# Performance work log

Measured on AMD Instinct MI355X. Metric: run time of the kernel, lower is better.

The kernel has to match this reference:

```python
import jax, jax.numpy as jnp
import numpy as np

B, T, C = 4, 2048, 1024
H, D = 16, 64           # num_heads, head_size
R = D // 2              # rotary_ndims = 32


def _make_rope(T, R):
    # RotaryEmbedding(dim=R): inv_freq over arange(0, R, 2)
    inv_freq = 1.0 / (10000.0 ** (np.arange(0, R, 2, dtype=np.float32) / R))
    t = np.arange(T, dtype=np.float32)
    freqs = np.einsum('i,j->ij', t, inv_freq)        # [T, R/2]
    emb = np.concatenate([freqs, freqs], axis=-1)    # [T, R]
    return jnp.asarray(np.stack([np.cos(emb), np.sin(emb)]), dtype=jnp.float32)  # [2, T, R]


def setup_inputs() -> dict:
    key = jax.random.key(0)
    ks = jax.random.split(key, 10)
    s = 1.0 / np.sqrt(C)
    inp = {
        'x': jax.random.normal(ks[0], (B, T, C), dtype=jnp.float32),
        'RoPE': _make_rope(T, R),
        'key_padding_mask': jax.random.randint(ks[1], (B, T), 0, 2, dtype=jnp.int32),
        'Wq': jax.random.normal(ks[2], (C, C), dtype=jnp.float32) * s,
        'bq': jnp.zeros((C,), dtype=jnp.float32),
        'Wk': jax.random.normal(ks[3], (C, C), dtype=jnp.float32) * s,
        'bk': jnp.zeros((C,), dtype=jnp.float32),
        'Wv': jax.random.normal(ks[4], (C, C), dtype=jnp.float32) * s,
        'bv': jnp.zeros((C,), dtype=jnp.float32),
        'Wo': jax.random.normal(ks[5], (C, C), dtype=jnp.float32) * s,
        'bo': jnp.zeros((C,), dtype=jnp.float32),
    }
    return inp


def _rotate_half(x):
    x1, x2 = x[..., : x.shape[-1] // 2], x[..., x.shape[-1] // 2:]
    return jnp.concatenate([-x2, x1], axis=-1)


def reference(x, RoPE, key_padding_mask, Wq, bq, Wk, bk, Wv, bv, Wo, bo):
    Bx, Tx, Cx = x.shape
    # projections -> [B, H, T, D]
    def proj(W, b):
        return (x @ W.T + b).reshape(Bx, Tx, H, D).transpose(0, 2, 1, 3)
    q, k, v = proj(Wq, bq), proj(Wk, bk), proj(Wv, bv)

    # partial rotary: first R dims rotated, rest passed through
    q_rot, q_pass = q[..., :R], q[..., R:]
    k_rot, k_pass = k[..., :R], k[..., R:]
    cos, sin = RoPE[0][:Tx], RoPE[1][:Tx]            # [T, R]
    q_rot = q_rot * cos + _rotate_half(q_rot) * sin
    k_rot = k_rot * cos + _rotate_half(k_rot) * sin
    q = jnp.concatenate([q_rot, q_pass], axis=-1)
    k = jnp.concatenate([k_rot, k_pass], axis=-1)

    att = jnp.einsum('bhqd,bhkd->bhqk', q, k) * (1.0 / np.sqrt(D))
    mask = key_padding_mask[:, None, None, :]        # [B,1,1,T]
    att = jnp.where(mask == 0, jnp.asarray(-1e30, att.dtype), att)
    att = jax.nn.softmax(att, axis=-1)
    out = jnp.einsum('bhqk,bhkd->bhqd', att, v)      # [B,H,T,D]
    out = out.transpose(0, 2, 1, 3).reshape(Bx, Tx, Cx)
    return out @ Wo.T + bo
```

## Files before the change

kernel.cpp:

```cpp
#include <hip/hip_runtime.h>
#include <stdint.h>


typedef __attribute__((ext_vector_type(8))) short bf16x8;
typedef __attribute__((ext_vector_type(4))) float f32x4;
typedef __attribute__((ext_vector_type(4))) short short4v;
typedef __attribute__((ext_vector_type(2))) uint32_t uint2v;

#define MFMA16(a, b, c) __builtin_amdgcn_mfma_f32_16x16x32_bf16((a), (b), (c), 0, 0, 0)

#if __has_builtin(__builtin_amdgcn_exp2f)
#define FEXP(x) __builtin_amdgcn_exp2f(x)
#define QSCALE 0.18033688011112042f
#else
#define FEXP(x) __expf(x)
#define QSCALE 0.125f
#endif

static __device__ __forceinline__ short f2bf(float f) {
  union { float fv; uint32_t u; } v; v.fv = f;
  uint32_t r = v.u + 0x7FFFu + ((v.u >> 16) & 1u);
  return (short)(r >> 16);
}

static __device__ __forceinline__ uint32_t pack_trunc(float a, float b) {
  union { float f; uint32_t u; } ua, ub;
  ua.f = a; ub.f = b;
#if __has_builtin(__builtin_amdgcn_perm)
  return __builtin_amdgcn_perm(ub.u, ua.u, 0x07060302u);
#else
  return (ub.u & 0xFFFF0000u) | (ua.u >> 16);
#endif
}

typedef __attribute__((address_space(1))) void as1_void;
typedef __attribute__((address_space(3))) void as3_void;
static __device__ __forceinline__ void gld_lds16(const void* g, void* l) {
  __builtin_amdgcn_global_load_lds((as1_void*)g, (as3_void*)l, 16, 0, 0);
}

__global__ __launch_bounds__(256) void cvt_kernel(
    const float* x, const float* wq, const float* wk, const float* wv,
    const float* wo,
    short* xb, short* wqb, short* wkb, short* wvb, short* wob) {
  int64_t g = (int64_t)blockIdx.x * 256 + threadIdx.x;
  const int64_t NX = 8388608 / 4, NW = 1048576 / 4;
  const float* src;
  short* dst;
  int64_t i;
  if (g < NX)               { src = x;  dst = xb;  i = g; }
  else if (g < NX + NW)     { src = wq; dst = wqb; i = g - NX; }
  else if (g < NX + 2 * NW) { src = wk; dst = wkb; i = g - NX - NW; }
  else if (g < NX + 3 * NW) { src = wv; dst = wvb; i = g - NX - 2 * NW; }
  else                      { src = wo; dst = wob; i = g - NX - 3 * NW; }
  float4 v = ((const float4*)src)[i];
  short4v o;
  o[0] = f2bf(v.x); o[1] = f2bf(v.y); o[2] = f2bf(v.z); o[3] = f2bf(v.w);
  *(short4v*)&dst[i * 4] = o;
}

__global__ __launch_bounds__(256) void qkv_gemm(
    const short* __restrict__ Xb,
    const short* __restrict__ Wq, const short* __restrict__ Wk,
    const short* __restrict__ Wv,
    const float* __restrict__ bq, const float* __restrict__ bk,
    const float* __restrict__ bv,
    const float* __restrict__ rope, const int* __restrict__ mask,
    short* __restrict__ Qh, short* __restrict__ Kh, short* __restrict__ Vt) {
  __shared__ __align__(16) short As[128 * 32];
  __shared__ __align__(16) short Bs[128 * 32];

  const int t = threadIdx.x;
  const int lane = t & 63;
  const int wave = t >> 6;
  const int c = lane & 15;
  const int quad = lane >> 4;
  const int m0 = blockIdx.x * 128;
  const int n0 = blockIdx.y * 128;
  const int mat = blockIdx.z;
  const short* Wg = (mat == 0) ? Wq : (mat == 1) ? Wk : Wv;
  const float* bias = (mat == 0) ? bq : (mat == 1) ? bk : bv;

  f32x4 zero4 = {0.f, 0.f, 0.f, 0.f};
  f32x4 acc[4][4];
#pragma unroll
  for (int i = 0; i < 4; ++i)
#pragma unroll
    for (int j = 0; j < 4; ++j) acc[i][j] = zero4;

  const int wm = wave & 1, wn = wave >> 1;

  const int srow = t >> 2;
  const int gc = ((t & 3) - (srow >> 2)) & 3;
  const short* gA = Xb + (size_t)(m0 + srow) * 1024 + gc * 8;
  const short* gB = Wg + (size_t)(n0 + srow) * 1024 + gc * 8;
  short* lA = &As[t * 8];
  short* lB = &Bs[t * 8];

  for (int k0 = 0; k0 < 1024; k0 += 32) {
    gld_lds16(gA + k0, lA);
    gld_lds16(gA + k0 + 65536, lA + 2048);
    gld_lds16(gB + k0, lB);
    gld_lds16(gB + k0 + 65536, lB + 2048);
    __syncthreads();

    bf16x8 af[4], bfr[4];
#pragma unroll
    for (int i = 0; i < 4; ++i) {
      int mr = wm * 64 + i * 16 + c;
      af[i] = *(const bf16x8*)&As[mr * 32 + (((quad + (mr >> 2)) & 3) * 8)];
      int nr = wn * 64 + i * 16 + c;
      bfr[i] = *(const bf16x8*)&Bs[nr * 32 + (((quad + (nr >> 2)) & 3) * 8)];
    }
#pragma unroll
    for (int i = 0; i < 4; ++i)
#pragma unroll
      for (int j = 0; j < 4; ++j) acc[i][j] = MFMA16(af[i], bfr[j], acc[i][j]);
    __syncthreads();
  }

  const int nb = n0 + wn * 64;
  const int hcol = nb >> 6;
  float bj[4];
#pragma unroll
  for (int j = 0; j < 4; ++j) bj[j] = bias[nb + j * 16 + c];
  const int bidx = m0 >> 11;
  const int tbase = (m0 & 2047) + wm * 64 + quad * 4;
  const int* mrow = mask + bidx * 2048;

  if (mat < 2) {
    short* Og = (mat == 0) ? Qh : Kh;
    size_t hb = (size_t)(bidx * 16 + hcol) * 2048;
#pragma unroll
    for (int i = 0; i < 4; ++i) {
#pragma unroll
      for (int r = 0; r < 4; ++r) {
        int tp = tbase + i * 16 + r;
        float f = (mat == 0) ? QSCALE : (mrow[tp] ? 1.0f : 0.0f);
        float cosv = rope[tp * 32 + c];
        float sinv = rope[65536 + tp * 32 + c];
        float v0 = acc[i][0][r] + bj[0];
        float v1 = acc[i][1][r] + bj[1];
        float v2 = acc[i][2][r] + bj[2];
        float v3 = acc[i][3][r] + bj[3];
        size_t base = (hb + tp) * 64;
        Og[base + c]      = f2bf((v0 * cosv - v1 * sinv) * f);
        Og[base + 16 + c] = f2bf((v1 * cosv + v0 * sinv) * f);
        Og[base + 32 + c] = f2bf(v2 * f);
        Og[base + 48 + c] = f2bf(v3 * f);
      }
    }
  } else {
    size_t hb = (size_t)(bidx * 16 + hcol) * 64;
#pragma unroll
    for (int i = 0; i < 4; ++i) {
      int tp = tbase + i * 16;
      int4 mv = *(const int4*)&mrow[tp];
      float fr[4];
      fr[0] = mv.x ? 1.f : 0.f; fr[1] = mv.y ? 1.f : 0.f;
      fr[2] = mv.z ? 1.f : 0.f; fr[3] = mv.w ? 1.f : 0.f;
#pragma unroll
      for (int j = 0; j < 4; ++j) {
        short4v pv;
#pragma unroll
        for (int r = 0; r < 4; ++r) pv[r] = f2bf((acc[i][j][r] + bj[j]) * fr[r]);
        size_t base = (hb + j * 16 + c) * 2048 + tp;
        *(short4v*)&Vt[base] = pv;
      }
    }
  }
}

__global__ __launch_bounds__(256, 2) void attn_kernel(
    const short* __restrict__ Qh, const short* __restrict__ Kh,
    const short* __restrict__ Vt, const int* __restrict__ mask,
    short* __restrict__ Og) {
  __shared__ __align__(16) short Ks[2][64 * 64];
  __shared__ __align__(16) short Vs[2][64 * 64];
  __shared__ __align__(16) short Pl[4][32 * 64];
  __shared__ float nmw[4];

  const int t = threadIdx.x;
  const int lane = t & 63;
  const int wave = t >> 6;
  const int c = lane & 15;
  const int quad = lane >> 4;
  const int qt = blockIdx.x;
  const int bh = blockIdx.y;
  const int bidx = bh >> 4;
  const short* Qg = Qh + ((size_t)bh * 2048 + qt * 256) * 64;
  const short* Kg = Kh + (size_t)bh * 2048 * 64;
  const short* Vg = Vt + (size_t)bh * 64 * 2048;

  {
    const int4* mr = (const int4*)(mask + bidx * 2048);
    int4 a = mr[t * 2], b = mr[t * 2 + 1];
    int cnt = (a.x == 0) + (a.y == 0) + (a.z == 0) + (a.w == 0) +
              (b.x == 0) + (b.y == 0) + (b.z == 0) + (b.w == 0);
    cnt += __shfl_xor(cnt, 1);  cnt += __shfl_xor(cnt, 2);
    cnt += __shfl_xor(cnt, 4);  cnt += __shfl_xor(cnt, 8);
    cnt += __shfl_xor(cnt, 16); cnt += __shfl_xor(cnt, 32);
    if (lane == 0) nmw[wave] = (float)cnt;
  }

  bf16x8 qf[2][4];
#pragma unroll
  for (int ks = 0; ks < 2; ++ks)
#pragma unroll
    for (int it = 0; it < 4; ++it)
      qf[ks][it] =
          *(const bf16x8*)&Qg[(wave * 64 + it * 16 + c) * 64 + ks * 32 + quad * 8];

  const bf16x8 ones = {0x3F80, 0x3F80, 0x3F80, 0x3F80,
                       0x3F80, 0x3F80, 0x3F80, 0x3F80};

  f32x4 zero4 = {0.f, 0.f, 0.f, 0.f};
  f32x4 O[4][4];
#pragma unroll
  for (int dt = 0; dt < 4; ++dt)
#pragma unroll
    for (int it = 0; it < 4; ++it) O[dt][it] = zero4;
  f32x4 Ol[4] = {zero4, zero4, zero4, zero4};

  const int krow0 = t >> 3;
  const int klc = (t & 7) ^ (krow0 & 7);
  const short* gk0 = Kg + (size_t)krow0 * 64 + klc * 8;
  const short* gv0 = Vg + (size_t)krow0 * 2048 + klc * 8;
  short* Pw = &Pl[wave][0];

  gld_lds16(gk0, &Ks[0][t * 8]);
  gld_lds16(gk0 + 32 * 64, &Ks[0][t * 8 + 2048]);
  gld_lds16(gv0, &Vs[0][t * 8]);
  gld_lds16(gv0 + 32 * 2048, &Vs[0][t * 8 + 2048]);

  for (int ci = 0; ci < 32; ++ci) {
    __syncthreads();
    if (ci < 31) {
      int cn = (ci + 1) * 64;
      int nb = (ci + 1) & 1;
      gld_lds16(gk0 + (size_t)cn * 64, &Ks[nb][t * 8]);
      gld_lds16(gk0 + (size_t)(cn + 32) * 64, &Ks[nb][t * 8 + 2048]);
      gld_lds16(gv0 + cn, &Vs[nb][t * 8]);
      gld_lds16(gv0 + cn + 32 * 2048, &Vs[nb][t * 8 + 2048]);
    }
    const short* ksb = &Ks[ci & 1][0];
    const short* vsb = &Vs[ci & 1][0];

#pragma unroll
    for (int h = 0; h < 2; ++h) {
      f32x4 St[4][2];
#pragma unroll
      for (int jt = 0; jt < 4; ++jt) {
        bf16x8 ak =
            *(const bf16x8*)&ksb[(jt * 16 + c) * 64 + ((quad ^ (c & 7)) * 8)];
        St[jt][0] = MFMA16(ak, qf[0][h * 2 + 0], zero4);
        St[jt][1] = MFMA16(ak, qf[0][h * 2 + 1], zero4);
      }
#pragma unroll
      for (int jt = 0; jt < 4; ++jt) {
        bf16x8 ak =
            *(const bf16x8*)&ksb[(jt * 16 + c) * 64 + (((4 + quad) ^ (c & 7)) * 8)];
        St[jt][0] = MFMA16(ak, qf[1][h * 2 + 0], St[jt][0]);
        St[jt][1] = MFMA16(ak, qf[1][h * 2 + 1], St[jt][1]);
      }

#pragma unroll
      for (int itl = 0; itl < 2; ++itl) {
#pragma unroll
        for (int jt = 0; jt < 4; ++jt) {
          float p0 = FEXP(St[jt][itl][0]);
          float p1 = FEXP(St[jt][itl][1]);
          float p2 = FEXP(St[jt][itl][2]);
          float p3 = FEXP(St[jt][itl][3]);
          uint2v pk;
          pk[0] = pack_trunc(p0, p1);
          pk[1] = pack_trunc(p2, p3);
          *(uint2v*)&Pw[(itl * 16 + c) * 64 +
                        (((jt * 2 + (quad >> 1)) ^ (c & 7)) * 8) +
                        (quad & 1) * 4] = pk;
        }
      }
      asm volatile("s_waitcnt lgkmcnt(0)" ::: "memory");

#pragma unroll
      for (int ks = 0; ks < 2; ++ks) {
        bf16x8 bp0 =
            *(const bf16x8*)&Pw[c * 64 + (((ks * 4 + quad) ^ (c & 7)) * 8)];
        bf16x8 bp1 =
            *(const bf16x8*)&Pw[(16 + c) * 64 + (((ks * 4 + quad) ^ (c & 7)) * 8)];
        Ol[h * 2 + 0] = MFMA16(ones, bp0, Ol[h * 2 + 0]);
        Ol[h * 2 + 1] = MFMA16(ones, bp1, Ol[h * 2 + 1]);
#pragma unroll
        for (int dt = 0; dt < 4; ++dt) {
          bf16x8 av =
              *(const bf16x8*)&vsb[(dt * 16 + c) * 64 + (((4 * ks + quad) ^ (c & 7)) * 8)];
          O[dt][h * 2 + 0] = MFMA16(av, bp0, O[dt][h * 2 + 0]);
          O[dt][h * 2 + 1] = MFMA16(av, bp1, O[dt][h * 2 + 1]);
        }
      }
    }
  }

  float nm = nmw[0] + nmw[1] + nmw[2] + nmw[3];
#pragma unroll
  for (int it = 0; it < 4; ++it) {
    float inv = 1.0f / (Ol[it][0] - nm);
    int tq = qt * 256 + wave * 64 + it * 16 + c;
    size_t rb = ((size_t)bidx * 2048 + tq) * 1024 + (size_t)(bh & 15) * 64;
#pragma unroll
    for (int dt = 0; dt < 4; ++dt) {
      short4v ov;
#pragma unroll
      for (int r = 0; r < 4; ++r) ov[r] = f2bf(O[dt][it][r] * inv);
      *(short4v*)&Og[rb + dt * 16 + quad * 4] = ov;
    }
  }
}

__global__ __launch_bounds__(256) void out_gemm(
    const short* __restrict__ Ab, const short* __restrict__ Wob,
    const float* __restrict__ bo, float* __restrict__ out) {
  __shared__ __align__(16) short As[64 * 32];
  __shared__ __align__(16) short Bs[128 * 32];

  const int t = threadIdx.x;
  const int lane = t & 63;
  const int wave = t >> 6;
  const int c = lane & 15;
  const int quad = lane >> 4;
  const int m0 = blockIdx.x * 64;
  const int n0 = blockIdx.y * 128;

  f32x4 zero4 = {0.f, 0.f, 0.f, 0.f};
  f32x4 acc[4][2];
#pragma unroll
  for (int i = 0; i < 4; ++i) {
    acc[i][0] = zero4;
    acc[i][1] = zero4;
  }

  const int srow = t >> 2;
  const int gc = ((t & 3) - (srow >> 2)) & 3;
  const short* gA = Ab + (size_t)(m0 + srow) * 1024 + gc * 8;
  const short* gB = Wob + (size_t)(n0 + srow) * 1024 + gc * 8;

  for (int k0 = 0; k0 < 1024; k0 += 32) {
    gld_lds16(gA + k0, &As[t * 8]);
    gld_lds16(gB + k0, &Bs[t * 8]);
    gld_lds16(gB + k0 + 65536, &Bs[t * 8 + 2048]);
    __syncthreads();

    bf16x8 af[4], bfr[2];
#pragma unroll
    for (int i = 0; i < 4; ++i) {
      int mr = i * 16 + c;
      af[i] = *(const bf16x8*)&As[mr * 32 + (((quad + (mr >> 2)) & 3) * 8)];
    }
#pragma unroll
    for (int j = 0; j < 2; ++j) {
      int nr = wave * 32 + j * 16 + c;
      bfr[j] = *(const bf16x8*)&Bs[nr * 32 + (((quad + (nr >> 2)) & 3) * 8)];
    }
#pragma unroll
    for (int i = 0; i < 4; ++i) {
      acc[i][0] = MFMA16(af[i], bfr[0], acc[i][0]);
      acc[i][1] = MFMA16(af[i], bfr[1], acc[i][1]);
    }
    __syncthreads();
  }

  const int nb = n0 + wave * 32;
  float bj[2];
  bj[0] = bo[nb + c];
  bj[1] = bo[nb + 16 + c];
#pragma unroll
  for (int i = 0; i < 4; ++i) {
    int m = m0 + i * 16 + quad * 4;
#pragma unroll
    for (int r = 0; r < 4; ++r) {
      float* orow = out + (size_t)(m + r) * 1024 + nb;
      orow[c]      = acc[i][0][r] + bj[0];
      orow[16 + c] = acc[i][1][r] + bj[1];
    }
  }
}

extern "C" void kernel_launch(void* const* d_in, const int* in_sizes, int n_in,
                              void* d_out, int out_size, void* d_ws,
                              size_t ws_size, hipStream_t stream) {
  const float* x    = (const float*)d_in[0];
  const float* rope = (const float*)d_in[1];
  const int*   mask = (const int*)d_in[2];
  const float* Wq   = (const float*)d_in[3];
  const float* bq   = (const float*)d_in[4];
  const float* Wk   = (const float*)d_in[5];
  const float* bk   = (const float*)d_in[6];
  const float* Wv   = (const float*)d_in[7];
  const float* bv   = (const float*)d_in[8];
  const float* Wo   = (const float*)d_in[9];
  const float* bo   = (const float*)d_in[10];
  float* out = (float*)d_out;

  char* ws = (char*)d_ws;
  short* xb  = (short*)(ws);
  short* wqb = (short*)(ws + 16777216);
  short* wkb = (short*)(ws + 18874368);
  short* wvb = (short*)(ws + 20971520);
  short* wob = (short*)(ws + 23068672);
  short* Qh  = (short*)(ws + 25198592);
  short* Kh  = (short*)(ws + 41975808);
  short* Vt  = (short*)(ws + 58753024);
  short* att = xb;

  cvt_kernel<<<12288, 256, 0, stream>>>(x, Wq, Wk, Wv, Wo, xb, wqb, wkb, wvb,
                                        wob);
  qkv_gemm<<<dim3(64, 8, 3), 256, 0, stream>>>(xb, wqb, wkb, wvb, bq, bk, bv,
                                               rope, mask, Qh, Kh, Vt);
  attn_kernel<<<dim3(8, 64), 256, 0, stream>>>(Qh, Kh, Vt, mask, att);
  out_gemm<<<dim3(128, 8), 256, 0, stream>>>(att, wob, bo, out);
}
```

Baseline: 298.9 us.

## Fuse Q/K/V GEMMs into one block sharing X tile, double-buffer GEMM loads

Each QKV block now computes all three projections for its 128x128 tile, so the X tile is loaded into shared memory once instead of three times. The block keeps three sets of accumulators, which cuts the grid to 512 blocks. Both the QKV and output GEMMs now double-buffer their shared-memory tiles, issuing the next K-slice's loads before computing the current one, with one barrier per iteration instead of two. The cost is 192 accumulator registers per thread, more shared memory per block and fewer blocks, which may lower occupancy or cause register spills.

```diff
diff --git a/kernel.cpp b/kernel.cpp
--- a/kernel.cpp
+++ b/kernel.cpp
@@ -59,7 +59,7 @@
   *(short4v*)&dst[i * 4] = o;
 }
 
-__global__ __launch_bounds__(256) void qkv_gemm(
+__global__ __launch_bounds__(256, 2) void qkv3_gemm(
     const short* __restrict__ Xb,
     const short* __restrict__ Wq, const short* __restrict__ Wk,
     const short* __restrict__ Wv,
@@ -67,8 +67,8 @@
     const float* __restrict__ bv,
     const float* __restrict__ rope, const int* __restrict__ mask,
     short* __restrict__ Qh, short* __restrict__ Kh, short* __restrict__ Vt) {
-  __shared__ __align__(16) short As[128 * 32];
-  __shared__ __align__(16) short Bs[128 * 32];
+  __shared__ __align__(16) short As[2][128 * 32];
+  __shared__ __align__(16) short Bs[2][3][128 * 32];
 
   const int t = threadIdx.x;
   const int lane = t & 63;
@@ -77,59 +77,81 @@
   const int quad = lane >> 4;
   const int m0 = blockIdx.x * 128;
   const int n0 = blockIdx.y * 128;
-  const int mat = blockIdx.z;
-  const short* Wg = (mat == 0) ? Wq : (mat == 1) ? Wk : Wv;
-  const float* bias = (mat == 0) ? bq : (mat == 1) ? bk : bv;
 
   f32x4 zero4 = {0.f, 0.f, 0.f, 0.f};
-  f32x4 acc[4][4];
-#pragma unroll
-  for (int i = 0; i < 4; ++i)
-#pragma unroll
-    for (int j = 0; j < 4; ++j) acc[i][j] = zero4;
+  f32x4 acc[3][4][4];
+#pragma unroll
+  for (int m = 0; m < 3; ++m)
+#pragma unroll
+    for (int i = 0; i < 4; ++i)
+#pragma unroll
+      for (int j = 0; j < 4; ++j) acc[m][i][j] = zero4;
 
   const int wm = wave & 1, wn = wave >> 1;
 
   const int srow = t >> 2;
   const int gc = ((t & 3) - (srow >> 2)) & 3;
   const short* gA = Xb + (size_t)(m0 + srow) * 1024 + gc * 8;
-  const short* gB = Wg + (size_t)(n0 + srow) * 1024 + gc * 8;
-  short* lA = &As[t * 8];
-  short* lB = &Bs[t * 8];
-
-  for (int k0 = 0; k0 < 1024; k0 += 32) {
-    gld_lds16(gA + k0, lA);
-    gld_lds16(gA + k0 + 65536, lA + 2048);
-    gld_lds16(gB + k0, lB);
-    gld_lds16(gB + k0 + 65536, lB + 2048);
+  const short* gW0 = Wq + (size_t)(n0 + srow) * 1024 + gc * 8;
+  const short* gW1 = Wk + (size_t)(n0 + srow) * 1024 + gc * 8;
+  const short* gW2 = Wv + (size_t)(n0 + srow) * 1024 + gc * 8;
+
+#define QKV_STAGE(buf, k0)                                  \
+  do {                                                      \
+    gld_lds16(gA + (k0), &As[buf][t * 8]);                  \
+    gld_lds16(gA + (k0) + 65536, &As[buf][t * 8 + 2048]);   \
+    gld_lds16(gW0 + (k0), &Bs[buf][0][t * 8]);              \
+    gld_lds16(gW0 + (k0) + 65536, &Bs[buf][0][t * 8 + 2048]); \
+    gld_lds16(gW1 + (k0), &Bs[buf][1][t * 8]);              \
+    gld_lds16(gW1 + (k0) + 65536, &Bs[buf][1][t * 8 + 2048]); \
+    gld_lds16(gW2 + (k0), &Bs[buf][2][t * 8]);              \
+    gld_lds16(gW2 + (k0) + 65536, &Bs[buf][2][t * 8 + 2048]); \
+  } while (0)
+
+  QKV_STAGE(0, 0);
+
+  for (int ki = 0; ki < 32; ++ki) {
     __syncthreads();
-
-    bf16x8 af[4], bfr[4];
+    if (ki < 31) QKV_STAGE((ki + 1) & 1, (ki + 1) * 32);
+
+    const short* as = &As[ki & 1][0];
+    bf16x8 af[4];
 #pragma unroll
     for (int i = 0; i < 4; ++i) {
       int mr = wm * 64 + i * 16 + c;
-      af[i] = *(const bf16x8*)&As[mr * 32 + (((quad + (mr >> 2)) & 3) * 8)];
-      int nr = wn * 64 + i * 16 + c;
-      bfr[i] = *(const bf16x8*)&Bs[nr * 32 + (((quad + (nr >> 2)) & 3) * 8)];
-    }
-#pragma unroll
-    for (int i = 0; i < 4; ++i)
-#pragma unroll
-      for (int j = 0; j < 4; ++j) acc[i][j] = MFMA16(af[i], bfr[j], acc[i][j]);
-    __syncthreads();
-  }
+      af[i] = *(const bf16x8*)&as[mr * 32 + (((quad + (mr >> 2)) & 3) * 8)];
+    }
+#pragma unroll
+    for (int m = 0; m < 3; ++m) {
+      const short* bs = &Bs[ki & 1][m][0];
+      bf16x8 bfr[4];
+#pragma unroll
+      for (int j = 0; j < 4; ++j) {
+        int nr = wn * 64 + j * 16 + c;
+        bfr[j] = *(const bf16x8*)&bs[nr * 32 + (((quad + (nr >> 2)) & 3) * 8)];
+      }
+#pragma unroll
+      for (int i = 0; i < 4; ++i)
+#pragma unroll
+        for (int j = 0; j < 4; ++j)
+          acc[m][i][j] = MFMA16(af[i], bfr[j], acc[m][i][j]);
+    }
+  }
+#undef QKV_STAGE
 
   const int nb = n0 + wn * 64;
   const int hcol = nb >> 6;
-  float bj[4];
-#pragma unroll
-  for (int j = 0; j < 4; ++j) bj[j] = bias[nb + j * 16 + c];
   const int bidx = m0 >> 11;
   const int tbase = (m0 & 2047) + wm * 64 + quad * 4;
   const int* mrow = mask + bidx * 2048;
 
-  if (mat < 2) {
+#pragma unroll
+  for (int mat = 0; mat < 2; ++mat) {
     short* Og = (mat == 0) ? Qh : Kh;
+    const float* bias = (mat == 0) ? bq : bk;
+    float bj[4];
+#pragma unroll
+    for (int j = 0; j < 4; ++j) bj[j] = bias[nb + j * 16 + c];
     size_t hb = (size_t)(bidx * 16 + hcol) * 2048;
 #pragma unroll
     for (int i = 0; i < 4; ++i) {
@@ -139,10 +161,10 @@
         float f = (mat == 0) ? QSCALE : (mrow[tp] ? 1.0f : 0.0f);
         float cosv = rope[tp * 32 + c];
         float sinv = rope[65536 + tp * 32 + c];
-        float v0 = acc[i][0][r] + bj[0];
-        float v1 = acc[i][1][r] + bj[1];
-        float v2 = acc[i][2][r] + bj[2];
-        float v3 = acc[i][3][r] + bj[3];
+        float v0 = acc[mat][i][0][r] + bj[0];
+        float v1 = acc[mat][i][1][r] + bj[1];
+        float v2 = acc[mat][i][2][r] + bj[2];
+        float v3 = acc[mat][i][3][r] + bj[3];
         size_t base = (hb + tp) * 64;
         Og[base + c]      = f2bf((v0 * cosv - v1 * sinv) * f);
         Og[base + 16 + c] = f2bf((v1 * cosv + v0 * sinv) * f);
@@ -150,7 +172,11 @@
         Og[base + 48 + c] = f2bf(v3 * f);
       }
     }
-  } else {
+  }
+  {
+    float bj[4];
+#pragma unroll
+    for (int j = 0; j < 4; ++j) bj[j] = bv[nb + j * 16 + c];
     size_t hb = (size_t)(bidx * 16 + hcol) * 64;
 #pragma unroll
     for (int i = 0; i < 4; ++i) {
@@ -163,7 +189,8 @@
       for (int j = 0; j < 4; ++j) {
         short4v pv;
 #pragma unroll
-        for (int r = 0; r < 4; ++r) pv[r] = f2bf((acc[i][j][r] + bj[j]) * fr[r]);
+        for (int r = 0; r < 4; ++r)
+          pv[r] = f2bf((acc[2][i][j][r] + bj[j]) * fr[r]);
         size_t base = (hb + j * 16 + c) * 2048 + tp;
         *(short4v*)&Vt[base] = pv;
       }
@@ -320,8 +347,8 @@
 __global__ __launch_bounds__(256) void out_gemm(
     const short* __restrict__ Ab, const short* __restrict__ Wob,
     const float* __restrict__ bo, float* __restrict__ out) {
-  __shared__ __align__(16) short As[64 * 32];
-  __shared__ __align__(16) short Bs[128 * 32];
+  __shared__ __align__(16) short As[2][64 * 32];
+  __shared__ __align__(16) short Bs[2][128 * 32];
 
   const int t = threadIdx.x;
   const int lane = t & 63;
@@ -344,30 +371,39 @@
   const short* gA = Ab + (size_t)(m0 + srow) * 1024 + gc * 8;
   const short* gB = Wob + (size_t)(n0 + srow) * 1024 + gc * 8;
 
-  for (int k0 = 0; k0 < 1024; k0 += 32) {
-    gld_lds16(gA + k0, &As[t * 8]);
-    gld_lds16(gB + k0, &Bs[t * 8]);
-    gld_lds16(gB + k0 + 65536, &Bs[t * 8 + 2048]);
+#define OUT_STAGE(buf, k0)                                   \
+  do {                                                       \
+    gld_lds16(gA + (k0), &As[buf][t * 8]);                   \
+    gld_lds16(gB + (k0), &Bs[buf][t * 8]);                   \
+    gld_lds16(gB + (k0) + 65536, &Bs[buf][t * 8 + 2048]);    \
+  } while (0)
+
+  OUT_STAGE(0, 0);
+
+  for (int ki = 0; ki < 32; ++ki) {
     __syncthreads();
-
+    if (ki < 31) OUT_STAGE((ki + 1) & 1, (ki + 1) * 32);
+
+    const short* as = &As[ki & 1][0];
+    const short* bs = &Bs[ki & 1][0];
     bf16x8 af[4], bfr[2];
 #pragma unroll
     for (int i = 0; i < 4; ++i) {
       int mr = i * 16 + c;
-      af[i] = *(const bf16x8*)&As[mr * 32 + (((quad + (mr >> 2)) & 3) * 8)];
+      af[i] = *(const bf16x8*)&as[mr * 32 + (((quad + (mr >> 2)) & 3) * 8)];
     }
 #pragma unroll
     for (int j = 0; j < 2; ++j) {
       int nr = wave * 32 + j * 16 + c;
-      bfr[j] = *(const bf16x8*)&Bs[nr * 32 + (((quad + (nr >> 2)) & 3) * 8)];
+      bfr[j] = *(const bf16x8*)&bs[nr * 32 + (((quad + (nr >> 2)) & 3) * 8)];
     }
 #pragma unroll
     for (int i = 0; i < 4; ++i) {
       acc[i][0] = MFMA16(af[i], bfr[0], acc[i][0]);
       acc[i][1] = MFMA16(af[i], bfr[1], acc[i][1]);
     }
-    __syncthreads();
-  }
+  }
+#undef OUT_STAGE
 
   const int nb = n0 + wave * 32;
   float bj[2];
@@ -414,8 +450,8 @@
 
   cvt_kernel<<<12288, 256, 0, stream>>>(x, Wq, Wk, Wv, Wo, xb, wqb, wkb, wvb,
                                         wob);
-  qkv_gemm<<<dim3(64, 8, 3), 256, 0, stream>>>(xb, wqb, wkb, wvb, bq, bk, bv,
-                                               rope, mask, Qh, Kh, Vt);
+  qkv3_gemm<<<dim3(64, 8), 256, 0, stream>>>(xb, wqb, wkb, wvb, bq, bk, bv,
+                                             rope, mask, Qh, Kh, Vt);
   attn_kernel<<<dim3(8, 64), 256, 0, stream>>>(Qh, Kh, Vt, mask, att);
   out_gemm<<<dim3(128, 8), 256, 0, stream>>>(att, wob, bo, out);
 }
```

After: 280.7 us. 6.1% less time.
